# Optimization experiments

Measured on AMD Instinct MI355X. Metric: run time of the kernel, lower is better.

The kernel has to match this reference:

```python
import jax, jax.numpy as jnp
import numpy as np

NY = NX = 256
NT = 256
B = 2
NSRC = 2
NREC = 64
DY = DX = 5.0
DT = 5e-4
PML = 20
PML_FREQ = 25.0


def setup_inputs() -> dict:
    key = jax.random.key(0)
    k1, k2, k3, k4, k5, k6 = jax.random.split(key, 6)
    # physically plausible elastic model
    vp = 3000.0 + 200.0 * jax.random.uniform(k1, (NY, NX), dtype=jnp.float32)
    vs = 1500.0 + 100.0 * jax.random.uniform(k2, (NY, NX), dtype=jnp.float32)
    rho = 2200.0 + 100.0 * jax.random.uniform(k3, (NY, NX), dtype=jnp.float32)
    lamb = rho * (vp ** 2 - 2.0 * vs ** 2)
    mu = rho * vs ** 2
    buoyancy = 1.0 / rho
    source_amplitudes_y = 1e3 * jax.random.normal(k4, (B, NSRC, NT), dtype=jnp.float32)
    lo, hi = PML + 10, NY - PML - 10  # keep sources/receivers inside the PML
    source_locations_y = jax.random.randint(k5, (B, NSRC, 2), lo, hi)
    receiver_locations_y = jax.random.randint(k6, (B, NREC, 2), lo, hi)
    return {
        "lamb": lamb,
        "mu": mu,
        "buoyancy": buoyancy,
        "source_amplitudes_y": source_amplitudes_y,
        "source_locations_y": source_locations_y,
        "receiver_locations_y": receiver_locations_y,
    }


def _pml_coeffs(n, width, dx, dt, max_vel, freq):
    # C-PML coefficients a, b along one axis; zero outside the PML region.
    i = jnp.arange(n, dtype=jnp.float32)
    frac = jnp.maximum(
        jnp.clip((width - i) / width, 0.0, 1.0),
        jnp.clip((i - (n - 1 - width)) / width, 0.0, 1.0),
    )
    sigma_max = 3.0 * max_vel * np.log(1000.0) / (2.0 * width * dx)
    sigma = sigma_max * frac ** 2
    alpha = np.pi * freq * (1.0 - frac)
    b = jnp.exp(-(sigma + alpha) * dt)
    a = sigma / (sigma + alpha + 1e-9) * (b - 1.0)
    return a, b


# staggered 2nd-order forward/backward differences (zero beyond the edge)
def _dfy(f):
    return jnp.pad(f[:, 1:] - f[:, :-1], ((0, 0), (0, 1), (0, 0))) / DY

def _dby(f):
    return jnp.pad(f[:, 1:] - f[:, :-1], ((0, 0), (1, 0), (0, 0))) / DY

def _dfx(f):
    return jnp.pad(f[:, :, 1:] - f[:, :, :-1], ((0, 0), (0, 0), (0, 1))) / DX

def _dbx(f):
    return jnp.pad(f[:, :, 1:] - f[:, :, :-1], ((0, 0), (0, 0), (1, 0))) / DX


def _forward(lamb, mu, buoyancy, amps, src_loc, rec_loc):
    ny, nx = lamb.shape
    bsz, nsrc, nt = amps.shape
    max_vel = jax.lax.stop_gradient(jnp.sqrt((lamb + 2.0 * mu) * buoyancy).max())
    ay, by = _pml_coeffs(ny, PML, DY, DT, max_vel, PML_FREQ)
    ax, bx = _pml_coeffs(nx, PML, DX, DT, max_vel, PML_FREQ)
    ay, by = ay[None, :, None], by[None, :, None]
    ax, bx = ax[None, None, :], bx[None, None, :]
    sb = jnp.arange(bsz)[:, None]
    sy, sx = src_loc[..., 0], src_loc[..., 1]
    ry, rx = rec_loc[..., 0], rec_loc[..., 1]
    src_scale = DT * buoyancy[sy, sx]  # [B, nsrc]
    l2m = lamb + 2.0 * mu
    z = jnp.zeros((bsz, ny, nx), lamb.dtype)
    fields0 = (z,) * 13  # vy, vx, syy, sxy, sxx + 8 PML memory fields

    def step(carry, amp_t):
        (vy, vx, syy, sxy, sxx,
         m_syyy, m_sxyx, m_sxyy, m_sxxx,
         m_vyy, m_vxx, m_vyx, m_vxy) = carry
        # velocity updates (with PML memory on stress derivatives)
        d = _dby(syy); m_syyy = by * m_syyy + ay * d; d_syy_y = d + m_syyy
        d = _dbx(sxy); m_sxyx = bx * m_sxyx + ax * d; d_sxy_x = d + m_sxyx
        vy = vy + DT * buoyancy * (d_syy_y + d_sxy_x)
        d = _dfy(sxy); m_sxyy = by * m_sxyy + ay * d; d_sxy_y = d + m_sxyy
        d = _dfx(sxx); m_sxxx = bx * m_sxxx + ax * d; d_sxx_x = d + m_sxxx
        vx = vx + DT * buoyancy * (d_sxy_y + d_sxx_x)
        # y-oriented source injection into vy
        vy = vy.at[sb, sy, sx].add(amp_t * src_scale)
        # stress updates (with PML memory on velocity derivatives)
        d = _dfy(vy); m_vyy = by * m_vyy + ay * d; d_vy_y = d + m_vyy
        d = _dbx(vx); m_vxx = bx * m_vxx + ax * d; d_vx_x = d + m_vxx
        syy = syy + DT * (l2m * d_vy_y + lamb * d_vx_x)
        sxx = sxx + DT * (lamb * d_vy_y + l2m * d_vx_x)
        d = _dbx(vy); m_vyx = bx * m_vyx + ax * d; d_vy_x = d + m_vyx
        d = _dby(vx); m_vxy = by * m_vxy + ay * d; d_vx_y = d + m_vxy
        sxy = sxy + DT * mu * (d_vy_x + d_vx_y)
        rec = vy[sb, ry, rx]  # [B, nrec]
        return (vy, vx, syy, sxy, sxx,
                m_syyy, m_sxyx, m_sxyy, m_sxxx,
                m_vyy, m_vxx, m_vyx, m_vxy), rec

    _, recs = jax.lax.scan(jax.checkpoint(step), fields0, jnp.transpose(amps, (2, 0, 1)))
    return jnp.transpose(recs, (1, 2, 0))  # [shot, receiver, time]


def reference(lamb, mu, buoyancy, source_amplitudes_y, source_locations_y, receiver_locations_y):
    return _forward(lamb, mu, buoyancy, source_amplitudes_y,
                    source_locations_y, receiver_locations_y)
```

## Files before the change

kernel.cpp:

```cpp
#include <hip/hip_runtime.h>

#define NYr 256
#define NXr 256
#define NTr 256
#define NBr 2
#define NSRCr 2
#define NRECr 64
#define NBLK 128
#define DTv 0.0005f
#define INVD 0.2f

#define COEF_OFF 0
#define FLAG_OFF 1024
#define STAGE_OFF 3072
#define STAGE_BLK (3*4*256)

__device__ __forceinline__ float ald(const float* p) {
  return __hip_atomic_load(p, __ATOMIC_RELAXED, __HIP_MEMORY_SCOPE_AGENT);
}
__device__ __forceinline__ void ast(float* p, float v) {
  __hip_atomic_store(p, v, __ATOMIC_RELAXED, __HIP_MEMORY_SCOPE_AGENT);
}

__global__ __launch_bounds__(256) void setup_kernel(
    const float* __restrict__ lamb, const float* __restrict__ mu,
    const float* __restrict__ buoy, float* __restrict__ coef)
{
  __shared__ float red[256];
  const int tid = threadIdx.x;
  float m = 0.0f;
  for (int i = tid; i < NYr*NXr; i += 256)
    m = fmaxf(m, sqrtf((lamb[i] + 2.0f*mu[i]) * buoy[i]));
  red[tid] = m;
  __syncthreads();
  for (int s = 128; s > 0; s >>= 1) {
    if (tid < s) red[tid] = fmaxf(red[tid], red[tid+s]);
    __syncthreads();
  }
  const float maxv = red[0];

  const float i_f = (float)tid;
  const float w = 20.0f;
  float f1 = fminf(fmaxf((w - i_f) * (1.0f/w), 0.0f), 1.0f);
  float f2 = fminf(fmaxf((i_f - (256.0f - 1.0f - w)) * (1.0f/w), 0.0f), 1.0f);
  float frac = fmaxf(f1, f2);
  float sigma_max = 3.0f * maxv * 6.907755278982137f / (2.0f * w * 5.0f);
  float sigma = sigma_max * frac * frac;
  float alpha = 3.14159265358979323f * 25.0f * (1.0f - frac);
  float bc = expf(-(sigma + alpha) * 0.0005f);
  float ac = sigma / (sigma + alpha + 1e-9f) * (bc - 1.0f);
  coef[tid]       = ac;
  coef[256 + tid] = bc;
  coef[512 + tid] = ac;
  coef[768 + tid] = bc;
}

__global__ __launch_bounds__(512) void elastic4(
    const float* __restrict__ lamb_g, const float* __restrict__ mu_g,
    const float* __restrict__ buoy_g, const float* __restrict__ amps,
    const int* __restrict__ src_loc, const int* __restrict__ rec_loc,
    float* __restrict__ ws, float* __restrict__ out)
{
  __shared__ float S[3][4][NXr];
  __shared__ float V[2][6][NXr];

  const int blk = blockIdx.x;
  const int b = blk >> 6, bi = blk & 63;
  const int tid = threadIdx.x;
  const int ty = tid >> 8, tx = tid & 255;
  const int lo = bi << 2;
  const bool hasUp = bi > 0, hasDn = bi < 63;

  const float* coef = ws + COEF_OFF;
  unsigned int* flags = (unsigned int*)(ws + FLAG_OFF);
  float* stage = ws + STAGE_OFF;

  const int txm = tx ? tx-1 : 0;
  const int txp = (tx < 255) ? tx+1 : 255;
  const bool xm_ok = tx > 0, xp_ok = tx < 255;
  const float axv = coef[512+tx], bxv = coef[768+tx];

  float vy_[3], vx_[3], myy[3], myx[3], mxyy[3], mxx[3];
  float dtb_[3], ayv[3], byv[3];
  #pragma unroll
  for (int k = 0; k < 3; ++k) {
    const int gy = lo - 1 + ty + 2*k;
    const bool ok = (gy >= 0) && (gy < NYr);
    const int gyc = ok ? gy : 0;
    dtb_[k] = ok ? DTv * buoy_g[gyc*NXr + tx] : 0.f;
    ayv[k]  = ok ? coef[gyc] : 0.f;
    byv[k]  = ok ? coef[256 + gyc] : 1.f;
    vy_[k] = vx_[k] = myy[k] = myx[k] = mxyy[k] = mxx[k] = 0.f;
  }
  float syy_[2], sxy_[2], sxx_[2], mvyy[2], mvxx[2], mvyx[2], mvxy[2];
  float lamv[2], muv[2], l2mv[2], ays[2], bys[2];
  #pragma unroll
  for (int j = 0; j < 2; ++j) {
    const int gy = lo + ty + 2*j;
    lamv[j] = lamb_g[gy*NXr + tx]; muv[j] = mu_g[gy*NXr + tx];
    l2mv[j] = lamv[j] + 2.f*muv[j];
    ays[j] = coef[gy]; bys[j] = coef[256 + gy];
    syy_[j] = sxy_[j] = sxx_[j] = 0.f;
    mvyy[j] = mvxx[j] = mvyx[j] = mvxy[j] = 0.f;
  }

  int sk0 = -1, sk1 = -1; int so0 = 0, so1 = 0;
  for (int i = 0; i < NBr*NSRCr; ++i) {
    const int sb = i >> 1, sy = src_loc[2*i], sx = src_loc[2*i+1];
    if (sb == b && sx == tx) {
      #pragma unroll
      for (int k = 0; k < 3; ++k) {
        const int gy = lo - 1 + ty + 2*k;
        if (gy == sy) { if (sk0 < 0) { sk0 = k; so0 = i*NTr; } else { sk1 = k; so1 = i*NTr; } }
      }
    }
  }
  const int gyA = ty ? lo     : lo + 1;
  const int gyB = ty ? lo + 2 : lo + 3;
  unsigned long long mA0=0, mA1=0, mB0=0, mB1=0;
  for (int i = 0; i < NBr*NRECr; ++i) {
    const int rb = i >> 6, ry = rec_loc[2*i], rx = rec_loc[2*i+1];
    if (rb == b && rx == tx) {
      if (ry == gyA) { if (i < 64) mA0 |= 1ull<<i; else mA1 |= 1ull<<(i-64); }
      if (ry == gyB) { if (i < 64) mB0 |= 1ull<<i; else mB1 |= 1ull<<(i-64); }
    }
  }
  const bool recA = (mA0|mA1) != 0ull, recB = (mB0|mB1) != 0ull;

  { float* p = &S[0][0][0]; for (int i = tid; i < 3*4*NXr; i += 512) p[i] = 0.f;
    float* q = &V[0][0][0]; for (int i = tid; i < 2*6*NXr; i += 512) q[i] = 0.f; }
  __syncthreads();

  for (int t = 0; t < NTr; ++t) {
    float a0 = 0.f, a1 = 0.f;
    if (sk0 >= 0) a0 = amps[so0 + t];
    if (sk1 >= 0) a1 = amps[so1 + t];

    {
      const int sr = 1 + ty;
      float d, u1, u2, u3, u4;
      d = (S[0][sr][tx] - S[0][sr-1][tx]) * INVD;
      myy[1] = byv[1]*myy[1] + ayv[1]*d; u1 = d + myy[1];
      d = xm_ok ? (S[1][sr][tx] - S[1][sr][txm]) * INVD : 0.f;
      myx[1] = bxv*myx[1] + axv*d; u2 = d + myx[1];
      vy_[1] += dtb_[1]*(u1+u2);
      d = (S[1][sr+1][tx] - S[1][sr][tx]) * INVD;
      mxyy[1] = byv[1]*mxyy[1] + ayv[1]*d; u3 = d + mxyy[1];
      d = xp_ok ? (S[2][sr][txp] - S[2][sr][tx]) * INVD : 0.f;
      mxx[1] = bxv*mxx[1] + axv*d; u4 = d + mxx[1];
      vx_[1] += dtb_[1]*(u3+u4);
      if (sk0 == 1) vy_[1] += a0*dtb_[1];
      if (sk1 == 1) vy_[1] += a1*dtb_[1];
      V[0][ty+2][tx] = vy_[1];
      V[1][ty+2][tx] = vx_[1];
    }

    if (t > 0) {
      const unsigned tgt = (unsigned)t;
      if (hasUp) { const unsigned int* f = &flags[(blk-1)*16];
        while (__hip_atomic_load(f, __ATOMIC_RELAXED, __HIP_MEMORY_SCOPE_AGENT) < tgt) {} }
      if (hasDn) { const unsigned int* f = &flags[(blk+1)*16];
        while (__hip_atomic_load(f, __ATOMIC_RELAXED, __HIP_MEMORY_SCOPE_AGENT) < tgt) {} }
    }
    asm volatile("" ::: "memory");

    const int pr = (t - 1) & 1;
    const float* up_sp = stage + (size_t)(pr*NBLK + (hasUp ? blk-1 : blk))*STAGE_BLK;
    const float* dn_sp = stage + (size_t)(pr*NBLK + (hasDn ? blk+1 : blk))*STAGE_BLK;

    if (ty == 0) {
      if (hasUp) {
        float syy2=0.f, syy3=0.f, sxy3t=0.f, sxy3m=0.f, sxx3t=0.f, sxx3p=0.f;
        if (t > 0) {
          syy2  = ald(up_sp + (0*4+2)*NXr + tx);
          syy3  = ald(up_sp + (0*4+3)*NXr + tx);
          sxy3t = ald(up_sp + (1*4+3)*NXr + tx);
          sxy3m = ald(up_sp + (1*4+3)*NXr + txm);
          sxx3t = ald(up_sp + (2*4+3)*NXr + tx);
          sxx3p = ald(up_sp + (2*4+3)*NXr + txp);
        }
        float d, u1, u2, u3, u4;
        d = (syy3 - syy2) * INVD;
        myy[0] = byv[0]*myy[0] + ayv[0]*d; u1 = d + myy[0];
        d = xm_ok ? (sxy3t - sxy3m) * INVD : 0.f;
        myx[0] = bxv*myx[0] + axv*d; u2 = d + myx[0];
        vy_[0] += dtb_[0]*(u1+u2);
        d = (S[1][0][tx] - sxy3t) * INVD;
        mxyy[0] = byv[0]*mxyy[0] + ayv[0]*d; u3 = d + mxyy[0];
        d = xp_ok ? (sxx3p - sxx3t) * INVD : 0.f;
        mxx[0] = bxv*mxx[0] + axv*d; u4 = d + mxx[0];
        vx_[0] += dtb_[0]*(u3+u4);
        if (sk0 == 0) vy_[0] += a0*dtb_[0];
        if (sk1 == 0) vy_[0] += a1*dtb_[0];
        V[0][0][tx] = vy_[0]; V[1][0][tx] = vx_[0];
      }
      {
        float sxy4t = (hasDn && t > 0) ? ald(dn_sp + (1*4+0)*NXr + tx) : 0.f;
        float d, u1, u2, u3, u4;
        d = (S[0][3][tx] - S[0][2][tx]) * INVD;
        myy[2] = byv[2]*myy[2] + ayv[2]*d; u1 = d + myy[2];
        d = xm_ok ? (S[1][3][tx] - S[1][3][txm]) * INVD : 0.f;
        myx[2] = bxv*myx[2] + axv*d; u2 = d + myx[2];
        vy_[2] += dtb_[2]*(u1+u2);
        d = hasDn ? (sxy4t - S[1][3][tx]) * INVD : 0.f;
        mxyy[2] = byv[2]*mxyy[2] + ayv[2]*d; u3 = d + mxyy[2];
        d = xp_ok ? (S[2][3][txp] - S[2][3][tx]) * INVD : 0.f;
        mxx[2] = bxv*mxx[2] + axv*d; u4 = d + mxx[2];
        vx_[2] += dtb_[2]*(u3+u4);
        if (sk0 == 2) vy_[2] += a0*dtb_[2];
        if (sk1 == 2) vy_[2] += a1*dtb_[2];
        V[0][4][tx] = vy_[2]; V[1][4][tx] = vx_[2];
      }
    } else {
      {
        float syyU = (hasUp && t > 0) ? ald(up_sp + (0*4+3)*NXr + tx) : 0.f;
        float d, u1, u2, u3, u4;
        d = hasUp ? (S[0][0][tx] - syyU) * INVD : 0.f;
        myy[0] = byv[0]*myy[0] + ayv[0]*d; u1 = d + myy[0];
        d = xm_ok ? (S[1][0][tx] - S[1][0][txm]) * INVD : 0.f;
        myx[0] = bxv*myx[0] + axv*d; u2 = d + myx[0];
        vy_[0] += dtb_[0]*(u1+u2);
        d = (S[1][1][tx] - S[1][0][tx]) * INVD;
        mxyy[0] = byv[0]*mxyy[0] + ayv[0]*d; u3 = d + mxyy[0];
        d = xp_ok ? (S[2][0][txp] - S[2][0][tx]) * INVD : 0.f;
        mxx[0] = bxv*mxx[0] + axv*d; u4 = d + mxx[0];
        vx_[0] += dtb_[0]*(u3+u4);
        if (sk0 == 0) vy_[0] += a0*dtb_[0];
        if (sk1 == 0) vy_[0] += a1*dtb_[0];
        V[0][1][tx] = vy_[0]; V[1][1][tx] = vx_[0];
      }
      if (hasDn) {
        float syyD0=0.f, sxyD0t=0.f, sxyD0m=0.f, sxyD1t=0.f, sxxD0t=0.f, sxxD0p=0.f;
        if (t > 0) {
          syyD0  = ald(dn_sp + (0*4+0)*NXr + tx);
          sxyD0t = ald(dn_sp + (1*4+0)*NXr + tx);
          sxyD0m = ald(dn_sp + (1*4+0)*NXr + txm);
          sxyD1t = ald(dn_sp + (1*4+1)*NXr + tx);
          sxxD0t = ald(dn_sp + (2*4+0)*NXr + tx);
          sxxD0p = ald(dn_sp + (2*4+0)*NXr + txp);
        }
        float d, u1, u2, u3, u4;
        d = (syyD0 - S[0][3][tx]) * INVD;
        myy[2] = byv[2]*myy[2] + ayv[2]*d; u1 = d + myy[2];
        d = xm_ok ? (sxyD0t - sxyD0m) * INVD : 0.f;
        myx[2] = bxv*myx[2] + axv*d; u2 = d + myx[2];
        vy_[2] += dtb_[2]*(u1+u2);
        d = (sxyD1t - sxyD0t) * INVD;
        mxyy[2] = byv[2]*mxyy[2] + ayv[2]*d; u3 = d + mxyy[2];
        d = xp_ok ? (sxxD0p - sxxD0t) * INVD : 0.f;
        mxx[2] = bxv*mxx[2] + axv*d; u4 = d + mxx[2];
        vx_[2] += dtb_[2]*(u3+u4);
        if (sk0 == 2) vy_[2] += a0*dtb_[2];
        if (sk1 == 2) vy_[2] += a1*dtb_[2];
        V[0][5][tx] = vy_[2]; V[1][5][tx] = vx_[2];
      }
    }

    if (recA) {
      const float v = ty ? vy_[0] : vy_[1];
      unsigned long long m = mA0; while (m) { int i = __ffsll((long long)m)-1; m &= m-1; out[i*NTr + t] = v; }
      m = mA1; while (m) { int i = __ffsll((long long)m)-1; m &= m-1; out[(i+64)*NTr + t] = v; }
    }
    if (recB) {
      const float v = ty ? vy_[1] : vy_[2];
      unsigned long long m = mB0; while (m) { int i = __ffsll((long long)m)-1; m &= m-1; out[i*NTr + t] = v; }
      m = mB1; while (m) { int i = __ffsll((long long)m)-1; m &= m-1; out[(i+64)*NTr + t] = v; }
    }

    __syncthreads();

    float* sp = stage + (size_t)((t & 1)*NBLK + blk)*STAGE_BLK;
    #pragma unroll
    for (int j = 0; j < 2; ++j) {
      const int gy = lo + ty + 2*j;
      const int vr = ty + 2*j + 1;
      float d, u5, u6, u7, u8;
      d = (gy < NYr-1) ? (V[0][vr+1][tx] - V[0][vr][tx]) * INVD : 0.f;
      mvyy[j] = bys[j]*mvyy[j] + ays[j]*d; u5 = d + mvyy[j];
      d = xm_ok ? (V[1][vr][tx] - V[1][vr][txm]) * INVD : 0.f;
      mvxx[j] = bxv*mvxx[j] + axv*d; u6 = d + mvxx[j];
      syy_[j] += DTv*(l2mv[j]*u5 + lamv[j]*u6);
      sxx_[j] += DTv*(lamv[j]*u5 + l2mv[j]*u6);
      d = xm_ok ? (V[0][vr][tx] - V[0][vr][txm]) * INVD : 0.f;
      mvyx[j] = bxv*mvyx[j] + axv*d; u7 = d + mvyx[j];
      d = (gy > 0) ? (V[1][vr][tx] - V[1][vr-1][tx]) * INVD : 0.f;
      mvxy[j] = bys[j]*mvxy[j] + ays[j]*d; u8 = d + mvxy[j];
      sxy_[j] += DTv*muv[j]*(u7 + u8);
      const int r = ty + 2*j;
      S[0][r][tx] = syy_[j]; S[1][r][tx] = sxy_[j]; S[2][r][tx] = sxx_[j];
      ast(sp + (0*4+r)*NXr + tx, syy_[j]);
      ast(sp + (1*4+r)*NXr + tx, sxy_[j]);
      ast(sp + (2*4+r)*NXr + tx, sxx_[j]);
    }
    __syncthreads();
    if (tid == 0)
      __hip_atomic_store(&flags[blk*16], (unsigned)(t+1),
                         __ATOMIC_RELAXED, __HIP_MEMORY_SCOPE_AGENT);
  }
}

extern "C" void kernel_launch(void* const* d_in, const int* in_sizes, int n_in,
                              void* d_out, int out_size, void* d_ws, size_t ws_size,
                              hipStream_t stream) {
  const float* lamb    = (const float*)d_in[0];
  const float* mu      = (const float*)d_in[1];
  const float* buoy    = (const float*)d_in[2];
  const float* amps    = (const float*)d_in[3];
  const int*   src_loc = (const int*)d_in[4];
  const int*   rec_loc = (const int*)d_in[5];
  float* out = (float*)d_out;
  float* ws  = (float*)d_ws;

  hipMemsetAsync(ws + FLAG_OFF, 0, NBLK*16*sizeof(unsigned int), stream);

  hipLaunchKernelGGL(setup_kernel, dim3(1), dim3(256), 0, stream,
                     lamb, mu, buoy, ws + COEF_OFF);

  void* args[] = { (void*)&lamb, (void*)&mu, (void*)&buoy, (void*)&amps,
                   (void*)&src_loc, (void*)&rec_loc, (void*)&ws, (void*)&out };
  hipLaunchCooperativeKernel((void*)elastic4, dim3(NBLK), dim3(512),
                             args, 0, stream);
}
```

Measured before the change: 762.8 us.

## Replace per-block flags with tagged 64-bit halo values for neighbor sync

Drops the per-block flag counters and the trailing syncthreads-then-flag-store handshake. Each halo stress value is now written as a 64-bit word that packs the float with a timestep tag, and consumers spin on the tags of exactly the words they need. Only the boundary rows neighbours read are published, which cuts staging writes. The aim is to remove the serialization of barrier plus flag store plus flag poll per step. In exchange every poll iteration costs more loads, and the memset now clears a much larger buffer.

```diff
diff --git a/kernel.cpp b/kernel.cpp
--- a/kernel.cpp
+++ b/kernel.cpp
@@ -11,16 +11,18 @@
 #define INVD 0.2f
 
 #define COEF_OFF 0
-#define FLAG_OFF 1024
-#define STAGE_OFF 3072
-#define STAGE_BLK (3*4*256)
-
-__device__ __forceinline__ float ald(const float* p) {
+#define TAG_F_OFF 1024
+#define TBLK 2048
+
+__device__ __forceinline__ unsigned long long tld(const unsigned long long* p) {
   return __hip_atomic_load(p, __ATOMIC_RELAXED, __HIP_MEMORY_SCOPE_AGENT);
 }
-__device__ __forceinline__ void ast(float* p, float v) {
-  __hip_atomic_store(p, v, __ATOMIC_RELAXED, __HIP_MEMORY_SCOPE_AGENT);
-}
+__device__ __forceinline__ void tst(unsigned long long* p, float v, unsigned tag) {
+  unsigned long long u = ((unsigned long long)tag << 32) | (unsigned long long)__float_as_uint(v);
+  __hip_atomic_store(p, u, __ATOMIC_RELAXED, __HIP_MEMORY_SCOPE_AGENT);
+}
+#define TVAL(x) __uint_as_float((unsigned)(x))
+#define TTAG(x) ((unsigned)((x) >> 32))
 
 __global__ __launch_bounds__(256) void setup_kernel(
     const float* __restrict__ lamb, const float* __restrict__ mu,
@@ -55,7 +57,7 @@
   coef[768 + tid] = bc;
 }
 
-__global__ __launch_bounds__(512) void elastic4(
+__global__ __launch_bounds__(512) void elastic_tag(
     const float* __restrict__ lamb_g, const float* __restrict__ mu_g,
     const float* __restrict__ buoy_g, const float* __restrict__ amps,
     const int* __restrict__ src_loc, const int* __restrict__ rec_loc,
@@ -72,8 +74,7 @@
   const bool hasUp = bi > 0, hasDn = bi < 63;
 
   const float* coef = ws + COEF_OFF;
-  unsigned int* flags = (unsigned int*)(ws + FLAG_OFF);
-  float* stage = ws + STAGE_OFF;
+  unsigned long long* tagb = (unsigned long long*)(ws + TAG_F_OFF);
 
   const int txm = tx ? tx-1 : 0;
   const int txp = (tx < 255) ? tx+1 : 255;
@@ -155,30 +156,41 @@
       V[1][ty+2][tx] = vx_[1];
     }
 
+    unsigned long long u4w=0, u5w=0, u6w=0, u6mw=0, u7w=0, u7pw=0;
+    unsigned long long d0w=0, d1w=0, d1mw=0, d2w=0, d3w=0, d3pw=0;
     if (t > 0) {
-      const unsigned tgt = (unsigned)t;
-      if (hasUp) { const unsigned int* f = &flags[(blk-1)*16];
-        while (__hip_atomic_load(f, __ATOMIC_RELAXED, __HIP_MEMORY_SCOPE_AGENT) < tgt) {} }
-      if (hasDn) { const unsigned int* f = &flags[(blk+1)*16];
-        while (__hip_atomic_load(f, __ATOMIC_RELAXED, __HIP_MEMORY_SCOPE_AGENT) < tgt) {} }
-    }
-    asm volatile("" ::: "memory");
-
-    const int pr = (t - 1) & 1;
-    const float* up_sp = stage + (size_t)(pr*NBLK + (hasUp ? blk-1 : blk))*STAGE_BLK;
-    const float* dn_sp = stage + (size_t)(pr*NBLK + (hasDn ? blk+1 : blk))*STAGE_BLK;
+      const size_t pslot = (size_t)((t-1)&1)*NBLK;
+      const unsigned long long* up = tagb + (pslot + (hasUp ? blk-1 : blk))*TBLK;
+      const unsigned long long* dn = tagb + (pslot + (hasDn ? blk+1 : blk))*TBLK;
+      const unsigned want = (unsigned)t;
+      if (ty == 0) {
+        for (;;) {
+          u4w = tld(up+4*256+tx); u5w = tld(up+5*256+tx); u6w = tld(up+6*256+tx);
+          u6mw = tld(up+6*256+txm); u7w = tld(up+7*256+tx); u7pw = tld(up+7*256+txp);
+          d1w = tld(dn+1*256+tx);
+          const bool okU = !hasUp || (TTAG(u4w)==want && TTAG(u5w)==want && TTAG(u6w)==want &&
+                                      TTAG(u6mw)==want && TTAG(u7w)==want && TTAG(u7pw)==want);
+          const bool okD = !hasDn || (TTAG(d1w)==want);
+          if (okU && okD) break;
+        }
+      } else {
+        for (;;) {
+          u5w = tld(up+5*256+tx);
+          d0w = tld(dn+0*256+tx); d1w = tld(dn+1*256+tx); d1mw = tld(dn+1*256+txm);
+          d2w = tld(dn+2*256+tx); d3w = tld(dn+3*256+tx); d3pw = tld(dn+3*256+txp);
+          const bool okU = !hasUp || (TTAG(u5w)==want);
+          const bool okD = !hasDn || (TTAG(d0w)==want && TTAG(d1w)==want && TTAG(d1mw)==want &&
+                                      TTAG(d2w)==want && TTAG(d3w)==want && TTAG(d3pw)==want);
+          if (okU && okD) break;
+        }
+      }
+    }
 
     if (ty == 0) {
       if (hasUp) {
-        float syy2=0.f, syy3=0.f, sxy3t=0.f, sxy3m=0.f, sxx3t=0.f, sxx3p=0.f;
-        if (t > 0) {
-          syy2  = ald(up_sp + (0*4+2)*NXr + tx);
-          syy3  = ald(up_sp + (0*4+3)*NXr + tx);
-          sxy3t = ald(up_sp + (1*4+3)*NXr + tx);
-          sxy3m = ald(up_sp + (1*4+3)*NXr + txm);
-          sxx3t = ald(up_sp + (2*4+3)*NXr + tx);
-          sxx3p = ald(up_sp + (2*4+3)*NXr + txp);
-        }
+        const float syy2 = TVAL(u4w), syy3 = TVAL(u5w);
+        const float sxy3t = TVAL(u6w), sxy3m = TVAL(u6mw);
+        const float sxx3t = TVAL(u7w), sxx3p = TVAL(u7pw);
         float d, u1, u2, u3, u4;
         d = (syy3 - syy2) * INVD;
         myy[0] = byv[0]*myy[0] + ayv[0]*d; u1 = d + myy[0];
@@ -195,7 +207,7 @@
         V[0][0][tx] = vy_[0]; V[1][0][tx] = vx_[0];
       }
       {
-        float sxy4t = (hasDn && t > 0) ? ald(dn_sp + (1*4+0)*NXr + tx) : 0.f;
+        const float sxy4t = TVAL(d1w);
         float d, u1, u2, u3, u4;
         d = (S[0][3][tx] - S[0][2][tx]) * INVD;
         myy[2] = byv[2]*myy[2] + ayv[2]*d; u1 = d + myy[2];
@@ -213,7 +225,7 @@
       }
     } else {
       {
-        float syyU = (hasUp && t > 0) ? ald(up_sp + (0*4+3)*NXr + tx) : 0.f;
+        const float syyU = TVAL(u5w);
         float d, u1, u2, u3, u4;
         d = hasUp ? (S[0][0][tx] - syyU) * INVD : 0.f;
         myy[0] = byv[0]*myy[0] + ayv[0]*d; u1 = d + myy[0];
@@ -230,15 +242,8 @@
         V[0][1][tx] = vy_[0]; V[1][1][tx] = vx_[0];
       }
       if (hasDn) {
-        float syyD0=0.f, sxyD0t=0.f, sxyD0m=0.f, sxyD1t=0.f, sxxD0t=0.f, sxxD0p=0.f;
-        if (t > 0) {
-          syyD0  = ald(dn_sp + (0*4+0)*NXr + tx);
-          sxyD0t = ald(dn_sp + (1*4+0)*NXr + tx);
-          sxyD0m = ald(dn_sp + (1*4+0)*NXr + txm);
-          sxyD1t = ald(dn_sp + (1*4+1)*NXr + tx);
-          sxxD0t = ald(dn_sp + (2*4+0)*NXr + tx);
-          sxxD0p = ald(dn_sp + (2*4+0)*NXr + txp);
-        }
+        const float syyD0 = TVAL(d0w), sxyD0t = TVAL(d1w), sxyD0m = TVAL(d1mw);
+        const float sxyD1t = TVAL(d2w), sxxD0t = TVAL(d3w), sxxD0p = TVAL(d3pw);
         float d, u1, u2, u3, u4;
         d = (syyD0 - S[0][3][tx]) * INVD;
         myy[2] = byv[2]*myy[2] + ayv[2]*d; u1 = d + myy[2];
@@ -269,7 +274,8 @@
 
     __syncthreads();
 
-    float* sp = stage + (size_t)((t & 1)*NBLK + blk)*STAGE_BLK;
+    unsigned long long* my = tagb + ((size_t)(t&1)*NBLK + blk)*TBLK;
+    const unsigned wtag = (unsigned)(t + 1);
     #pragma unroll
     for (int j = 0; j < 2; ++j) {
       const int gy = lo + ty + 2*j;
@@ -287,15 +293,22 @@
       mvxy[j] = bys[j]*mvxy[j] + ays[j]*d; u8 = d + mvxy[j];
       sxy_[j] += DTv*muv[j]*(u7 + u8);
       const int r = ty + 2*j;
+      if (r == 0) {
+        tst(my + 0*256 + tx, syy_[j], wtag);
+        tst(my + 1*256 + tx, sxy_[j], wtag);
+        tst(my + 3*256 + tx, sxx_[j], wtag);
+      } else if (r == 1) {
+        tst(my + 2*256 + tx, sxy_[j], wtag);
+      } else if (r == 2) {
+        tst(my + 4*256 + tx, syy_[j], wtag);
+      } else {
+        tst(my + 5*256 + tx, syy_[j], wtag);
+        tst(my + 6*256 + tx, sxy_[j], wtag);
+        tst(my + 7*256 + tx, sxx_[j], wtag);
+      }
       S[0][r][tx] = syy_[j]; S[1][r][tx] = sxy_[j]; S[2][r][tx] = sxx_[j];
-      ast(sp + (0*4+r)*NXr + tx, syy_[j]);
-      ast(sp + (1*4+r)*NXr + tx, sxy_[j]);
-      ast(sp + (2*4+r)*NXr + tx, sxx_[j]);
     }
     __syncthreads();
-    if (tid == 0)
-      __hip_atomic_store(&flags[blk*16], (unsigned)(t+1),
-                         __ATOMIC_RELAXED, __HIP_MEMORY_SCOPE_AGENT);
   }
 }
 
@@ -311,13 +324,14 @@
   float* out = (float*)d_out;
   float* ws  = (float*)d_ws;
 
-  hipMemsetAsync(ws + FLAG_OFF, 0, NBLK*16*sizeof(unsigned int), stream);
+  hipMemsetAsync((char*)ws + TAG_F_OFF*sizeof(float), 0,
+                 (size_t)2*NBLK*TBLK*sizeof(unsigned long long), stream);
 
   hipLaunchKernelGGL(setup_kernel, dim3(1), dim3(256), 0, stream,
                      lamb, mu, buoy, ws + COEF_OFF);
 
   void* args[] = { (void*)&lamb, (void*)&mu, (void*)&buoy, (void*)&amps,
                    (void*)&src_loc, (void*)&rec_loc, (void*)&ws, (void*)&out };
-  hipLaunchCooperativeKernel((void*)elastic4, dim3(NBLK), dim3(512),
+  hipLaunchCooperativeKernel((void*)elastic_tag, dim3(NBLK), dim3(512),
                              args, 0, stream);
 }
```

New measurement: 671.6 us. 1.14x faster.
